# Optimization experiments

Hardware: AMD Instinct MI355X
Metric: run time of the kernel (lower is better)

Reference implementation:

```python
import jax, jax.numpy as jnp
import numpy as np
from jax import lax

B = 16384
ENC_LEN = 48
ENC_HID = 128   # 2 * enc_dim (bidirectional)
DEC_DIM = 32
IN_DIM = 4
T_DEC = 12


def setup_inputs() -> dict:
    key = jax.random.key(0)
    ks = jax.random.split(key, 12)
    f32 = jnp.float32
    return {
        "y": jax.random.normal(ks[0], (B, 13, IN_DIM), f32),
        "encoder_outputs": jax.random.normal(ks[1], (ENC_LEN, B, ENC_HID), f32),
        "hidden": jax.random.normal(ks[2], (B, DEC_DIM), f32),
        "batch_ids": jax.random.randint(ks[3], (B,), 0, 1000),
        "attn_W": jax.random.normal(ks[4], (ENC_LEN, IN_DIM + DEC_DIM), f32) * 0.1,
        "attn_b": jnp.zeros((ENC_LEN,), f32),
        "comb_W": jax.random.normal(ks[5], (IN_DIM, IN_DIM + ENC_HID), f32) * 0.1,
        "comb_b": jnp.zeros((IN_DIM,), f32),
        "w_ih": jax.random.normal(ks[6], (3 * DEC_DIM, IN_DIM), f32) * 0.1,
        "w_hh": jax.random.normal(ks[7], (3 * DEC_DIM, DEC_DIM), f32) * 0.1,
        "b_ih": jnp.zeros((3 * DEC_DIM,), f32),
        "b_hh": jnp.zeros((3 * DEC_DIM,), f32),
        "fc_W": jax.random.normal(ks[8], (1, DEC_DIM), f32) * 0.1,
        "fc_b": jnp.zeros((1,), f32),
    }


def _gru_cell(x, h, w_ih, w_hh, b_ih, b_hh):
    # torch GRU gate ordering: r, z, n
    gi = x @ w_ih.T + b_ih          # (B, 3*DEC_DIM)
    gh = h @ w_hh.T + b_hh
    i_r, i_z, i_n = jnp.split(gi, 3, axis=1)
    h_r, h_z, h_n = jnp.split(gh, 3, axis=1)
    r = jax.nn.sigmoid(i_r + h_r)
    z = jax.nn.sigmoid(i_z + h_z)
    n = jnp.tanh(i_n + r * h_n)
    return (1.0 - z) * n + z * h


def reference(y, encoder_outputs, hidden, batch_ids, attn_W, attn_b,
              comb_W, comb_b, w_ih, w_hh, b_ih, b_hh, fc_W, fc_b):
    # y: (B, 13, 4) -> y_: (13, B, 4); encoder_outputs: (ENC_LEN, B, 128) -> (B, ENC_LEN, 128)
    y_ = jnp.transpose(y, (1, 0, 2))
    enc = jnp.transpose(encoder_outputs, (1, 0, 2))
    x0 = jnp.nan_to_num(y_[0])  # rnn_input[rnn_input != rnn_input] = 0
    # dropout(p=0.5) treated as identity (eval mode)

    def step(carry, y_next3):
        x, h = carry  # x: (B, IN_DIM), h: (B, DEC_DIM)
        # Bahdanau-ish attention: softmax over enc_len positions
        attn_logits = jnp.concatenate([x, h], axis=1) @ attn_W.T + attn_b  # (B, ENC_LEN)
        aw = jax.nn.softmax(attn_logits, axis=1)
        ctx = jnp.einsum('be,bed->bd', aw, enc)  # (B, ENC_HID)
        x2 = jnp.concatenate([ctx, x], axis=1) @ comb_W.T + comb_b  # (B, IN_DIM)
        h = _gru_cell(x2, h, w_ih, w_hh, b_ih, b_hh)
        out = h @ fc_W.T + fc_b  # (B, 1)
        x_next = jnp.concatenate([y_next3, out], axis=1)  # (B, IN_DIM)
        return (x_next, h), out

    xs = y_[1:13, :, 1:]  # (12, B, 3): next-step exogenous features
    (_, _), outs = lax.scan(step, (x0, hidden), xs)  # outs: (12, B, 1)
    y_pred = outs[:, :, 0]  # cat(dim=1).transpose(0,1) -> (12, B)
    return y_pred
```

## Files before the change

### kernel.cpp

```cpp
#include <hip/hip_runtime.h>

#define B 16384
#define ENC_LEN 48
#define ENC_HID 128
#define T_DEC 12

#define NWAVE 16
#define EPW 3
#define UPW 2

__device__ __forceinline__ float fast_rcp(float x) { return __builtin_amdgcn_rcpf(x); }
__device__ __forceinline__ float fast_exp(float x) { return __expf(x); }
__device__ __forceinline__ float sigmoidf_(float x) { return fast_rcp(1.f + fast_exp(-x)); }
__device__ __forceinline__ float tanhf_(float x) {
    return 1.f - 2.f * fast_rcp(1.f + fast_exp(2.f * x));
}
__device__ __forceinline__ float nan_to_num_(float v) { return (v != v) ? 0.f : v; }

__global__ __launch_bounds__(256) void precompute_P_kernel(
    const float* __restrict__ enc,
    const float* __restrict__ cW,
    float4* __restrict__ P)
{
    const int l = threadIdx.x & 7;
    const int rowLocal = threadIdx.x >> 3;

    float w[4][4][4];
    #pragma unroll
    for (int i = 0; i < 4; ++i)
        #pragma unroll
        for (int k = 0; k < 4; ++k) {
            float4 t = *(const float4*)(cW + i * 132 + k * 32 + l * 4);
            w[i][k][0] = t.x; w[i][k][1] = t.y; w[i][k][2] = t.z; w[i][k][3] = t.w;
        }

    const int totalRows = ENC_LEN * B;
    const int stride = gridDim.x * 32;
    for (int row = blockIdx.x * 32 + rowLocal; row < totalRows; row += stride) {
        const float* r = enc + (size_t)row * ENC_HID;
        float4 e[4];
        #pragma unroll
        for (int k = 0; k < 4; ++k)
            e[k] = *(const float4*)(r + k * 32 + l * 4);

        float a[4];
        #pragma unroll
        for (int i = 0; i < 4; ++i) {
            float s0 = e[0].x * w[i][0][0] + e[0].y * w[i][0][1] + e[0].z * w[i][0][2] + e[0].w * w[i][0][3];
            float s1 = e[1].x * w[i][1][0] + e[1].y * w[i][1][1] + e[1].z * w[i][1][2] + e[1].w * w[i][1][3];
            float s2 = e[2].x * w[i][2][0] + e[2].y * w[i][2][1] + e[2].z * w[i][2][2] + e[2].w * w[i][2][3];
            float s3 = e[3].x * w[i][3][0] + e[3].y * w[i][3][1] + e[3].z * w[i][3][2] + e[3].w * w[i][3][3];
            a[i] = (s0 + s1) + (s2 + s3);
        }
        #pragma unroll
        for (int m = 1; m < 8; m <<= 1) {
            #pragma unroll
            for (int i = 0; i < 4; ++i)
                a[i] += __shfl_xor(a[i], m, 8);
        }
        if (l == 0) P[row] = make_float4(a[0], a[1], a[2], a[3]);
    }
}

__global__ __launch_bounds__(1024, 4) void decode_kernel(
    const float* __restrict__ y,
    const float* __restrict__ hidden,
    const float4* __restrict__ P,
    const float* __restrict__ aW,
    const float* __restrict__ ab,
    const float* __restrict__ cW,
    const float* __restrict__ cb,
    const float* __restrict__ wih,
    const float* __restrict__ whh,
    const float* __restrict__ bih,
    const float* __restrict__ bhh,
    const float* __restrict__ fW,
    const float* __restrict__ fb,
    float* __restrict__ out)
{
    __shared__ float sh_h[64 * 36];
    __shared__ float sh_red[2][64][6];

    const int lane = threadIdx.x & 63;
    const int w = __builtin_amdgcn_readfirstlane(threadIdx.x >> 6);
    const int b = blockIdx.x * 64 + lane;

    {
        float2 v = *(const float2*)(hidden + (size_t)b * 32 + w * 2);
        *(float2*)(&sh_h[lane * 36 + w * 2]) = v;
    }
    for (int i = threadIdx.x; i < 2 * 64 * 6; i += 1024)
        (&sh_red[0][0][0])[i] = 0.f;

    float4 pb[EPW];
    #pragma unroll
    for (int i = 0; i < EPW; ++i)
        pb[i] = P[(size_t)(w * EPW + i) * B + b];

    float xA[4];
    #pragma unroll
    for (int k = 0; k < 4; ++k)
        xA[k] = nan_to_num_(y[(size_t)b * 52 + k]);

    __syncthreads();

    for (int t = 0; t < T_DEC; ++t) {
        const int buf = t & 1;

        float h[32];
        #pragma unroll
        for (int k = 0; k < 8; ++k) {
            float4 v = *(const float4*)(&sh_h[lane * 36 + k * 4]);
            h[k * 4 + 0] = v.x; h[k * 4 + 1] = v.y; h[k * 4 + 2] = v.z; h[k * 4 + 3] = v.w;
        }

        float Sp = 0.f, c0 = 0.f, c1 = 0.f, c2 = 0.f, c3 = 0.f;
        #pragma unroll
        for (int i = 0; i < EPW; ++i) {
            const int e = w * EPW + i;
            const float* wr = aW + e * 36;
            float s = ab[e] + wr[0] * xA[0] + wr[1] * xA[1] + wr[2] * xA[2] + wr[3] * xA[3];
            #pragma unroll
            for (int j = 0; j < 32; ++j) s += wr[4 + j] * h[j];
            float g = fast_exp(s);
            Sp += g;
            c0 += g * pb[i].x; c1 += g * pb[i].y; c2 += g * pb[i].z; c3 += g * pb[i].w;
        }
        atomicAdd(&sh_red[buf][lane][0], Sp);
        atomicAdd(&sh_red[buf][lane][1], c0);
        atomicAdd(&sh_red[buf][lane][2], c1);
        atomicAdd(&sh_red[buf][lane][3], c2);
        atomicAdd(&sh_red[buf][lane][4], c3);

        __syncthreads();

        const float S  = sh_red[buf][lane][0];
        const float rs = fast_rcp(S);
        float x2g[4];
        #pragma unroll
        for (int i = 0; i < 4; ++i) {
            const float* cr = cW + i * 132 + 128;
            x2g[i] = sh_red[buf][lane][1 + i] * rs
                   + cr[0] * xA[0] + cr[1] * xA[1] + cr[2] * xA[2] + cr[3] * xA[3] + cb[i];
        }
        if (w == 0) {
            #pragma unroll
            for (int k = 0; k < 6; ++k) sh_red[buf ^ 1][lane][k] = 0.f;
        }

        float hn[UPW];
        #pragma unroll
        for (int u = 0; u < UPW; ++u) {
            const int g = w * UPW + u;
            float ir = bih[g], iz = bih[g + 32], in_ = bih[g + 64];
            #pragma unroll
            for (int k = 0; k < 4; ++k) {
                ir  += wih[g * 4 + k]        * x2g[k];
                iz  += wih[(g + 32) * 4 + k] * x2g[k];
                in_ += wih[(g + 64) * 4 + k] * x2g[k];
            }
            float hr = bhh[g], hz = bhh[g + 32], hn_ = bhh[g + 64];
            #pragma unroll
            for (int k = 0; k < 32; ++k) {
                hr  += whh[g * 32 + k]        * h[k];
                hz  += whh[(g + 32) * 32 + k] * h[k];
                hn_ += whh[(g + 64) * 32 + k] * h[k];
            }
            float r = sigmoidf_(ir + hr);
            float z = sigmoidf_(iz + hz);
            float n = tanhf_(in_ + r * hn_);
            hn[u] = (1.f - z) * n + z * h[g];
        }
        *(float2*)(&sh_h[lane * 36 + w * UPW]) = make_float2(hn[0], hn[1]);

        atomicAdd(&sh_red[buf][lane][5], fW[w * UPW] * hn[0] + fW[w * UPW + 1] * hn[1]);

        __syncthreads();

        const float o = sh_red[buf][lane][5] + fb[0];
        if (w == 0) out[t * B + b] = o;

        if (t < T_DEC - 1) {
            float4 yv = *(const float4*)(y + (size_t)b * 52 + (t + 1) * 4);
            xA[0] = yv.y; xA[1] = yv.z; xA[2] = yv.w; xA[3] = o;
        }
    }
}

extern "C" void kernel_launch(void* const* d_in, const int* in_sizes, int n_in,
                              void* d_out, int out_size, void* d_ws, size_t ws_size,
                              hipStream_t stream)
{
    const float* y   = (const float*)d_in[0];
    const float* enc = (const float*)d_in[1];
    const float* hid = (const float*)d_in[2];
    const float* aW  = (const float*)d_in[4];
    const float* ab  = (const float*)d_in[5];
    const float* cW  = (const float*)d_in[6];
    const float* cb  = (const float*)d_in[7];
    const float* wih = (const float*)d_in[8];
    const float* whh = (const float*)d_in[9];
    const float* bih = (const float*)d_in[10];
    const float* bhh = (const float*)d_in[11];
    const float* fW  = (const float*)d_in[12];
    const float* fb  = (const float*)d_in[13];
    float* out = (float*)d_out;

    float4* P = (float4*)d_ws;

    precompute_P_kernel<<<4096, 256, 0, stream>>>(enc, cW, P);
    decode_kernel<<<B / 64, 1024, 0, stream>>>(
        y, hid, P, aW, ab, cW, cb, wih, whh, bih, bhh, fW, fb, out);
}
```

Baseline: 698.6 us.

## Remap decode to 16 batch rows per 256-thread block with shuffle reductions

The decode kernel now gives each block 16 batch rows with 256 threads, splitting each wave into four 16-lane groups that each own different attention positions and GRU units. Cross-group partial sums are combined with xor shuffles first, so only 16 lanes per wave issue LDS atomics. Weight reads are vectorised as float4 dot products. The goal is to cut LDS atomic contention and the cost of 1024-thread barriers. In exchange, weight loads are no longer wave-uniform: lanes in one wave read different weight rows, which may turn scalar loads into vector loads.

```diff
diff --git a/kernel.cpp b/kernel.cpp
--- a/kernel.cpp
+++ b/kernel.cpp
@@ -4,10 +4,6 @@
 #define ENC_LEN 48
 #define ENC_HID 128
 #define T_DEC 12
-
-#define NWAVE 16
-#define EPW 3
-#define UPW 2
 
 __device__ __forceinline__ float fast_rcp(float x) { return __builtin_amdgcn_rcpf(x); }
 __device__ __forceinline__ float fast_exp(float x) { return __expf(x); }
@@ -16,6 +12,9 @@
     return 1.f - 2.f * fast_rcp(1.f + fast_exp(2.f * x));
 }
 __device__ __forceinline__ float nan_to_num_(float v) { return (v != v) ? 0.f : v; }
+__device__ __forceinline__ float dot4(float4 a, const float* v) {
+    return a.x * v[0] + a.y * v[1] + a.z * v[2] + a.w * v[3];
+}
 
 __global__ __launch_bounds__(256) void precompute_P_kernel(
     const float* __restrict__ enc,
@@ -62,7 +61,7 @@
     }
 }
 
-__global__ __launch_bounds__(1024, 4) void decode_kernel(
+__global__ __launch_bounds__(256, 4) void decode_kernel(
     const float* __restrict__ y,
     const float* __restrict__ hidden,
     const float4* __restrict__ P,
@@ -78,29 +77,33 @@
     const float* __restrict__ fb,
     float* __restrict__ out)
 {
-    __shared__ float sh_h[64 * 36];
-    __shared__ float sh_red[2][64][6];
-
-    const int lane = threadIdx.x & 63;
-    const int w = __builtin_amdgcn_readfirstlane(threadIdx.x >> 6);
-    const int b = blockIdx.x * 64 + lane;
+    __shared__ float sh_h[16][36];
+    __shared__ float sh_red[2][16][8];
+
+    const int tid  = threadIdx.x;
+    const int lane = tid & 63;
+    const int bl   = lane & 15;
+    const int sub  = (tid >> 6) * 4 + (lane >> 4);
+    const int gb   = blockIdx.x * 16 + bl;
+    const int g0   = sub * 2;
 
     {
-        float2 v = *(const float2*)(hidden + (size_t)b * 32 + w * 2);
-        *(float2*)(&sh_h[lane * 36 + w * 2]) = v;
-    }
-    for (int i = threadIdx.x; i < 2 * 64 * 6; i += 1024)
-        (&sh_red[0][0][0])[i] = 0.f;
-
-    float4 pb[EPW];
+        float2 v = *(const float2*)(hidden + (size_t)gb * 32 + g0);
+        *(float2*)(&sh_h[bl][g0]) = v;
+    }
+    (&sh_red[0][0][0])[tid] = 0.f;
+
+    float4 pb[3];
     #pragma unroll
-    for (int i = 0; i < EPW; ++i)
-        pb[i] = P[(size_t)(w * EPW + i) * B + b];
+    for (int i = 0; i < 3; ++i)
+        pb[i] = P[(size_t)(sub * 3 + i) * B + gb];
 
     float xA[4];
-    #pragma unroll
-    for (int k = 0; k < 4; ++k)
-        xA[k] = nan_to_num_(y[(size_t)b * 52 + k]);
+    {
+        float4 yv = *(const float4*)(y + (size_t)gb * 52);
+        xA[0] = nan_to_num_(yv.x); xA[1] = nan_to_num_(yv.y);
+        xA[2] = nan_to_num_(yv.z); xA[3] = nan_to_num_(yv.w);
+    }
 
     __syncthreads();
 
@@ -110,78 +113,100 @@
         float h[32];
         #pragma unroll
         for (int k = 0; k < 8; ++k) {
-            float4 v = *(const float4*)(&sh_h[lane * 36 + k * 4]);
-            h[k * 4 + 0] = v.x; h[k * 4 + 1] = v.y; h[k * 4 + 2] = v.z; h[k * 4 + 3] = v.w;
+            float4 v = *(const float4*)(&sh_h[bl][k * 4]);
+            h[4 * k + 0] = v.x; h[4 * k + 1] = v.y; h[4 * k + 2] = v.z; h[4 * k + 3] = v.w;
         }
 
         float Sp = 0.f, c0 = 0.f, c1 = 0.f, c2 = 0.f, c3 = 0.f;
         #pragma unroll
-        for (int i = 0; i < EPW; ++i) {
-            const int e = w * EPW + i;
-            const float* wr = aW + e * 36;
-            float s = ab[e] + wr[0] * xA[0] + wr[1] * xA[1] + wr[2] * xA[2] + wr[3] * xA[3];
+        for (int i = 0; i < 3; ++i) {
+            const int e = sub * 3 + i;
+            const float4* wr = (const float4*)(aW + e * 36);
+            float s = ab[e] + dot4(wr[0], xA);
             #pragma unroll
-            for (int j = 0; j < 32; ++j) s += wr[4 + j] * h[j];
+            for (int q = 0; q < 8; ++q)
+                s += dot4(wr[1 + q], h + 4 * q);
             float g = fast_exp(s);
             Sp += g;
             c0 += g * pb[i].x; c1 += g * pb[i].y; c2 += g * pb[i].z; c3 += g * pb[i].w;
         }
-        atomicAdd(&sh_red[buf][lane][0], Sp);
-        atomicAdd(&sh_red[buf][lane][1], c0);
-        atomicAdd(&sh_red[buf][lane][2], c1);
-        atomicAdd(&sh_red[buf][lane][3], c2);
-        atomicAdd(&sh_red[buf][lane][4], c3);
+        #pragma unroll
+        for (int m = 16; m < 64; m <<= 1) {
+            Sp += __shfl_xor(Sp, m);
+            c0 += __shfl_xor(c0, m); c1 += __shfl_xor(c1, m);
+            c2 += __shfl_xor(c2, m); c3 += __shfl_xor(c3, m);
+        }
+        if (lane < 16) {
+            atomicAdd(&sh_red[buf][bl][0], Sp);
+            atomicAdd(&sh_red[buf][bl][1], c0);
+            atomicAdd(&sh_red[buf][bl][2], c1);
+            atomicAdd(&sh_red[buf][bl][3], c2);
+            atomicAdd(&sh_red[buf][bl][4], c3);
+        }
 
         __syncthreads();
 
-        const float S  = sh_red[buf][lane][0];
-        const float rs = fast_rcp(S);
-        float x2g[4];
+        const float rs = fast_rcp(sh_red[buf][bl][0]);
+        float x2v[4];
         #pragma unroll
         for (int i = 0; i < 4; ++i) {
             const float* cr = cW + i * 132 + 128;
-            x2g[i] = sh_red[buf][lane][1 + i] * rs
+            x2v[i] = sh_red[buf][bl][1 + i] * rs
                    + cr[0] * xA[0] + cr[1] * xA[1] + cr[2] * xA[2] + cr[3] * xA[3] + cb[i];
         }
-        if (w == 0) {
-            #pragma unroll
-            for (int k = 0; k < 6; ++k) sh_red[buf ^ 1][lane][k] = 0.f;
-        }
-
-        float hn[UPW];
-        #pragma unroll
-        for (int u = 0; u < UPW; ++u) {
-            const int g = w * UPW + u;
-            float ir = bih[g], iz = bih[g + 32], in_ = bih[g + 64];
-            #pragma unroll
-            for (int k = 0; k < 4; ++k) {
-                ir  += wih[g * 4 + k]        * x2g[k];
-                iz  += wih[(g + 32) * 4 + k] * x2g[k];
-                in_ += wih[(g + 64) * 4 + k] * x2g[k];
-            }
-            float hr = bhh[g], hz = bhh[g + 32], hn_ = bhh[g + 64];
-            #pragma unroll
-            for (int k = 0; k < 32; ++k) {
-                hr  += whh[g * 32 + k]        * h[k];
-                hz  += whh[(g + 32) * 32 + k] * h[k];
-                hn_ += whh[(g + 64) * 32 + k] * h[k];
-            }
-            float r = sigmoidf_(ir + hr);
-            float z = sigmoidf_(iz + hz);
-            float n = tanhf_(in_ + r * hn_);
-            hn[u] = (1.f - z) * n + z * h[g];
-        }
-        *(float2*)(&sh_h[lane * 36 + w * UPW]) = make_float2(hn[0], hn[1]);
-
-        atomicAdd(&sh_red[buf][lane][5], fW[w * UPW] * hn[0] + fW[w * UPW + 1] * hn[1]);
+        if (tid < 128) {
+            (&sh_red[buf ^ 1][0][0])[tid] = 0.f;
+        }
+
+        float2 bir = *(const float2*)(bih + g0);
+        float2 biz = *(const float2*)(bih + 32 + g0);
+        float2 bin = *(const float2*)(bih + 64 + g0);
+        float ir0 = bir.x + dot4(*(const float4*)(wih + (g0)      * 4), x2v);
+        float ir1 = bir.y + dot4(*(const float4*)(wih + (g0 + 1)  * 4), x2v);
+        float iz0 = biz.x + dot4(*(const float4*)(wih + (g0 + 32) * 4), x2v);
+        float iz1 = biz.y + dot4(*(const float4*)(wih + (g0 + 33) * 4), x2v);
+        float in0 = bin.x + dot4(*(const float4*)(wih + (g0 + 64) * 4), x2v);
+        float in1 = bin.y + dot4(*(const float4*)(wih + (g0 + 65) * 4), x2v);
+
+        float2 bhr = *(const float2*)(bhh + g0);
+        float2 bhz = *(const float2*)(bhh + 32 + g0);
+        float2 bhn = *(const float2*)(bhh + 64 + g0);
+        float hr0 = bhr.x, hr1 = bhr.y, hz0 = bhz.x, hz1 = bhz.y, hn0 = bhn.x, hn1 = bhn.y;
+        const float* w0 = whh + (size_t)(g0)      * 32;
+        const float* w1 = whh + (size_t)(g0 + 1)  * 32;
+        const float* w2 = whh + (size_t)(g0 + 32) * 32;
+        const float* w3 = whh + (size_t)(g0 + 33) * 32;
+        const float* w4 = whh + (size_t)(g0 + 64) * 32;
+        const float* w5 = whh + (size_t)(g0 + 65) * 32;
+        #pragma unroll
+        for (int q = 0; q < 8; ++q) {
+            const float* hq = h + 4 * q;
+            hr0 += dot4(*(const float4*)(w0 + 4 * q), hq);
+            hr1 += dot4(*(const float4*)(w1 + 4 * q), hq);
+            hz0 += dot4(*(const float4*)(w2 + 4 * q), hq);
+            hz1 += dot4(*(const float4*)(w3 + 4 * q), hq);
+            hn0 += dot4(*(const float4*)(w4 + 4 * q), hq);
+            hn1 += dot4(*(const float4*)(w5 + 4 * q), hq);
+        }
+        float r0 = sigmoidf_(ir0 + hr0), r1 = sigmoidf_(ir1 + hr1);
+        float z0 = sigmoidf_(iz0 + hz0), z1 = sigmoidf_(iz1 + hz1);
+        float n0 = tanhf_(in0 + r0 * hn0), n1 = tanhf_(in1 + r1 * hn1);
+        float hw0 = (1.f - z0) * n0 + z0 * h[g0];
+        float hw1 = (1.f - z1) * n1 + z1 * h[g0 + 1];
+        *(float2*)(&sh_h[bl][g0]) = make_float2(hw0, hw1);
+
+        float fcp = fW[g0] * hw0 + fW[g0 + 1] * hw1;
+        #pragma unroll
+        for (int m = 16; m < 64; m <<= 1) fcp += __shfl_xor(fcp, m);
+        if (lane < 16) atomicAdd(&sh_red[buf][bl][5], fcp);
 
         __syncthreads();
 
-        const float o = sh_red[buf][lane][5] + fb[0];
-        if (w == 0) out[t * B + b] = o;
+        const float o = sh_red[buf][bl][5] + fb[0];
+        if (tid < 16) out[t * B + gb] = o;
 
         if (t < T_DEC - 1) {
-            float4 yv = *(const float4*)(y + (size_t)b * 52 + (t + 1) * 4);
+            float4 yv = *(const float4*)(y + (size_t)gb * 52 + (t + 1) * 4);
             xA[0] = yv.y; xA[1] = yv.z; xA[2] = yv.w; xA[3] = o;
         }
     }
@@ -209,6 +234,6 @@
     float4* P = (float4*)d_ws;
 
     precompute_P_kernel<<<4096, 256, 0, stream>>>(enc, cW, P);
-    decode_kernel<<<B / 64, 1024, 0, stream>>>(
+    decode_kernel<<<B / 16, 256, 0, stream>>>(
         y, hid, P, aW, ab, cW, cb, wih, whh, bih, bhh, fW, fb, out);
 }
```

After: 1.309 ms. 1.87x slower.
